# Kernel optimization log

Hardware: AMD Instinct MI355X
Metric: run time of the kernel (lower is better)

Reference implementation:

```python
import jax, jax.numpy as jnp
import numpy as np

INPUT_DIM = 512
LATENT_DIM = 64
H1, H2 = 128, 64  # hardcoded hidden widths in Encoder/Decoder
BATCH = 4096


def _xavier(key, shape):
    fan_out, fan_in = shape
    std = jnp.sqrt(2.0 / (fan_in + fan_out))
    return std * jax.random.normal(key, shape, dtype=jnp.float32)


def setup_inputs() -> dict:
    key = jax.random.key(0)
    ks = jax.random.split(key, 10)
    d = LATENT_DIM
    n_pairs = d * (d - 1) // 2
    n_funcs = 1 + d + n_pairs  # bias + states + pairwise products
    inp = {
        "x": jax.random.normal(ks[0], (BATCH, INPUT_DIM), dtype=jnp.float32),
        "xdot": jax.random.normal(ks[1], (BATCH, INPUT_DIM), dtype=jnp.float32),
        # encoder weights (torch Linear layout: [out, in])
        "We1": _xavier(ks[2], (H1, INPUT_DIM)), "be1": jnp.zeros((H1,), jnp.float32),
        "We2": _xavier(ks[3], (H2, H1)),        "be2": jnp.zeros((H2,), jnp.float32),
        "We3": _xavier(ks[4], (d, H2)),         "be3": jnp.zeros((d,), jnp.float32),
        # decoder weights
        "Wd1": _xavier(ks[5], (H2, d)),         "bd1": jnp.zeros((H2,), jnp.float32),
        "Wd2": _xavier(ks[6], (H1, H2)),        "bd2": jnp.zeros((H1,), jnp.float32),
        "Wd3": _xavier(ks[7], (INPUT_DIM, H1)), "bd3": jnp.zeros((INPUT_DIM,), jnp.float32),
        "XI": jnp.ones((n_funcs, d), jnp.float32),
        "XI_mask": jnp.ones((n_funcs, d), jnp.float32),
    }
    return inp


def _mlp_with_jacobian(x, Ws, bs):
    """3-layer relu MLP; returns output and per-sample analytic Jacobian [B,out,in].
    Jacobian = diag(m3) W3 diag(m2) W2 diag(m1) W1 with relu masks m_l."""
    h = x
    J = None
    for W, b in zip(Ws, bs):
        h = h @ W.T + b                      # [B, out_l]
        m = (h > 0).astype(h.dtype)          # relu mask (grad 0 at 0, matching torch)
        h = jnp.maximum(h, 0)
        Wm = m[:, :, None] * W[None]         # [B, out_l, in_l]
        J = Wm if J is None else jnp.einsum('boh,bhi->boi', Wm, J)
    return h, J


def _sindy_library(z):
    B, d = z.shape
    iu, ju = np.triu_indices(d, k=1)
    ones = jnp.ones((B, 1), z.dtype)
    pairs = z[:, iu] * z[:, ju]              # [B, d(d-1)/2]
    return jnp.concatenate([ones, z, pairs], axis=1)


def reference(x, xdot, We1, be1, We2, be2, We3, be3,
              Wd1, bd1, Wd2, bd2, Wd3, bd3, XI, XI_mask):
    z, Jenc = _mlp_with_jacobian(x, (We1, We2, We3), (be1, be2, be3))
    dz_dt = jnp.einsum('bli,bi->bl', Jenc, xdot)
    xh, Jdec = _mlp_with_jacobian(z, (Wd1, Wd2, Wd3), (bd1, bd2, bd3))
    theta = _sindy_library(z)
    dz_dt_sindy = theta @ (XI_mask * XI)
    dxh_dt = jnp.einsum('bol,bl->bo', Jdec, dz_dt_sindy)
    return (xh, dxh_dt, z, dz_dt, dz_dt_sindy)
```

## Files before the change

### kernel.cpp

```cpp
#include <hip/hip_runtime.h>

#define BATCH 4096
#define IN_DIM 512
#define H1DIM 128
#define H2DIM 64
#define DDIM 64
#define NFUNC 2081
#define NFPAD 2112
#define CHUNK 704
#define KS_PER_CHUNK 22

typedef short bf16x8 __attribute__((ext_vector_type(8)));
typedef float f32x4 __attribute__((ext_vector_type(4)));
#define MFMA(a,b,c) __builtin_amdgcn_mfma_f32_16x16x32_bf16(a,b,c,0,0,0)

#define WSZ1 (H1DIM*IN_DIM)
#define WSZ2 (H2DIM*H1DIM)
#define WSZ3 (DDIM*H2DIM)
#define WSZ4 (H2DIM*DDIM)
#define WSZ5 (H1DIM*H2DIM)
#define WSZ6 (IN_DIM*H1DIM)

__device__ __forceinline__ short f2b(float f) {
    union { float f; unsigned u; } x; x.f = f;
    unsigned r = x.u + 0x7fffu + ((x.u >> 16) & 1u);
    return (short)(r >> 16);
}
__device__ __forceinline__ float b2f(short s) {
    union { unsigned u; float f; } x; x.u = ((unsigned)(unsigned short)s) << 16;
    return x.f;
}
__device__ __forceinline__ void split3f(float v, short& s0, short& s1, short& s2) {
    s0 = f2b(v); float r = v - b2f(s0);
    s1 = f2b(r); float r2 = r - b2f(s1);
    s2 = f2b(r2);
}
__device__ __forceinline__ uint2 pk4(const short* s) {
    union { short s[4]; uint2 u; } z;
    z.s[0] = s[0]; z.s[1] = s[1]; z.s[2] = s[2]; z.s[3] = s[3];
    return z.u;
}

template<int N> __device__ __forceinline__ void waitv() {
    asm volatile("s_waitcnt vmcnt(%0)" :: "n"(N) : "memory");
    __builtin_amdgcn_sched_barrier(0);
}

__device__ __forceinline__ void st_b16(short* t, int RS, int r, int c, short v) {
    int b = (c * 2) ^ ((r & 7) << 4);
    *(short*)((char*)(t + r * RS) + b) = v;
}
__device__ __forceinline__ void st_b64(short* t, int RS, int r, int c0, uint2 v) {
    int b = (c0 * 2) ^ ((r & 7) << 4);
    *(uint2*)((char*)(t + r * RS) + b) = v;
}
__device__ __forceinline__ bf16x8 ld_af(const short* t, int RS, int lane, int kbase) {
    int r = lane & 15;
    int b = ((kbase + (lane >> 4) * 8) * 2) ^ ((r & 7) << 4);
    return *(const bf16x8*)((const char*)(t + r * RS) + b);
}
__device__ __forceinline__ bf16x8 ld_bp(const short* P, int blk, int lane) {
    return *(const bf16x8*)(P + ((size_t)blk * 64 + lane) * 8);
}

__device__ __forceinline__ void mf9(bf16x8 f0, bf16x8 f1, bf16x8 f2, bf16x8 fv,
                                    bf16x8 b0, bf16x8 b1, bf16x8 b2,
                                    f32x4& P, f32x4& Q, f32x4& V) {
    P = MFMA(f0, b0, P); Q = MFMA(f1, b1, Q);
    P = MFMA(f1, b0, P); Q = MFMA(f0, b1, Q);
    P = MFMA(f2, b0, P); Q = MFMA(f2, b1, Q);
    P = MFMA(f0, b2, P); Q = MFMA(f1, b2, Q);
    V = MFMA(fv, b0, V);
}

__device__ __forceinline__ void epi_store(short* t0, short* t1, short* t2, short* tv, int RS,
                                          int lane, int col, const f32x4& P, const f32x4& Q,
                                          const f32x4& V, float bb)
{
    #pragma unroll
    for (int q = 0; q < 4; ++q) {
        int row = (lane >> 4) * 4 + q;
        float pre = P[q] + Q[q] + bb;
        float h = fmaxf(pre, 0.f);
        short s0, s1, s2;
        split3f(h, s0, s1, s2);
        st_b16(t0, RS, row, col, s0);
        st_b16(t1, RS, row, col, s1);
        st_b16(t2, RS, row, col, s2);
        st_b16(tv, RS, row, col, pre > 0.f ? f2b(V[q]) : (short)0);
    }
}

template<int K>
__device__ void pack_w(const float* __restrict__ W, short* __restrict__ dst, int NK,
                       int gid, int nthr)
{
    for (int i = gid; i < NK; i += nthr) {
        int c = i / K, k = i % K;
        int cb = c >> 4, ks = k >> 5;
        int L = (((k >> 3) & 3) << 4) | (c & 15);
        int j = k & 7;
        int idx = ((cb * (K / 32) + ks) * 64 + L) * 8 + j;
        short s0, s1, s2; split3f(W[i], s0, s1, s2);
        dst[idx] = s0; dst[idx + NK] = s1; dst[idx + 2 * NK] = s2;
    }
}

__global__ void initk(const float* __restrict__ x, const float* __restrict__ xdot,
                      const float* __restrict__ We1, const float* __restrict__ We2,
                      const float* __restrict__ We3, const float* __restrict__ Wd1,
                      const float* __restrict__ Wd2, const float* __restrict__ Wd3,
                      const float* __restrict__ XI, const float* __restrict__ XIm,
                      float* __restrict__ xh, float* __restrict__ dxh,
                      short* Wp1, short* Wp2, short* Wp3, short* Wp4, short* Wp5, short* Wp6,
                      short* xiP, int2* pk)
{
    int gid = blockIdx.x * blockDim.x + threadIdx.x;
    int nthr = gridDim.x * blockDim.x;

    for (int i = gid; i < (BATCH / 16) * 16 * 64; i += nthr) {
        int L = i & 63, ks = (i >> 6) & 15, rb = i >> 10;
        int row = rb * 16 + (L & 15);
        int k0 = ks * 32 + ((L >> 4) << 3);
        const float* px = &x[(size_t)row * IN_DIM + k0];
        const float* pd = &xdot[(size_t)row * IN_DIM + k0];
        union { short s[8]; bf16x8 v; } a0, a1, a2, dv;
        #pragma unroll
        for (int j = 0; j < 8; ++j) {
            split3f(px[j], a0.s[j], a1.s[j], a2.s[j]);
            dv.s[j] = f2b(pd[j]);
        }
        short* bx = (short*)(xh + (size_t)rb * 8192);
        short* bd = (short*)(dxh + (size_t)rb * 8192);
        int off = (ks * 64 + L) * 8;
        *(bf16x8*)(bx + off) = a0.v;
        *(bf16x8*)(bx + 8192 + off) = a1.v;
        *(bf16x8*)(bd + off) = a2.v;
        *(bf16x8*)(bd + 8192 + off) = dv.v;
    }

    pack_w<512>(We1, Wp1, WSZ1, gid, nthr);
    pack_w<128>(We2, Wp2, WSZ2, gid, nthr);
    pack_w<64>(We3, Wp3, WSZ3, gid, nthr);
    pack_w<64>(Wd1, Wp4, WSZ4, gid, nthr);
    pack_w<64>(Wd2, Wp5, WSZ5, gid, nthr);
    pack_w<128>(Wd3, Wp6, WSZ6, gid, nthr);

    for (int i = gid; i < 4 * 66 * 64; i += nthr) {
        int cb = i / (66 * 64);
        int r = i - cb * (66 * 64);
        int ks = r >> 6, L = r & 63;
        int col = cb * 16 + (L & 15);
        union { short s[8]; bf16x8 v; } w;
        #pragma unroll
        for (int j = 0; j < 8; ++j) {
            int f = ks * 32 + ((L >> 4) << 3) + j;
            float v = (f < NFUNC) ? XI[(size_t)f * DDIM + col] * XIm[(size_t)f * DDIM + col] : 0.f;
            w.s[j] = f2b(v);
        }
        *(bf16x8*)(xiP + (size_t)i * 8) = w.v;
    }

    for (int f = gid; f < NFPAD; f += nthr) {
        int a, b;
        if (f == 0) { a = 64; b = 64; }
        else if (f <= DDIM) { a = f - 1; b = 64; }
        else if (f < NFUNC) {
            int p = f - 1 - DDIM; int i2 = 0, cum = 0;
            while (cum + (63 - i2) <= p) { cum += 63 - i2; ++i2; }
            a = i2; b = i2 + 1 + (p - cum);
        } else { a = 65; b = 65; }
        pk[f] = make_int2(a, b);
    }
}

__global__ __launch_bounds__(256, 1)
void fused(const float* __restrict__ be1, const float* __restrict__ be2,
           const float* __restrict__ be3, const float* __restrict__ bd1,
           const float* __restrict__ bd2, const float* __restrict__ bd3,
           const short* __restrict__ Wp1, const short* __restrict__ Wp2,
           const short* __restrict__ Wp3, const short* __restrict__ Wp4,
           const short* __restrict__ Wp5, const short* __restrict__ Wp6,
           const short* __restrict__ xiP, const int2* __restrict__ pk,
           float* __restrict__ xh, float* __restrict__ dxh, float* __restrict__ zo,
           float* __restrict__ dz, float* __restrict__ dzs)
{
    __shared__ __align__(1024) char lds[122880];
#define GLL(gp, lo) __builtin_amdgcn_global_load_lds( \
        (const __attribute__((address_space(1))) unsigned int*)(gp), \
        (__attribute__((address_space(3))) unsigned int*)&lds[lo], 16, 0, 0)

    short* h1s0 = (short*)(lds + 0);
    short* h1s1 = (short*)(lds + 4096);
    short* h1s2 = (short*)(lds + 8192);
    short* v1   = (short*)(lds + 12288);
    short* h2s0 = (short*)(lds + 16384);
    short* h2s1 = (short*)(lds + 18432);
    short* h2s2 = (short*)(lds + 20480);
    short* v2   = (short*)(lds + 22528);
    short* th   = (short*)(lds + 0);
    short* g1s0 = (short*)(lds + 0);
    short* g1s1 = (short*)(lds + 2048);
    short* g1s2 = (short*)(lds + 4096);
    short* u1   = (short*)(lds + 6144);
    short* g2s0 = (short*)(lds + 8192);
    short* g2s1 = (short*)(lds + 12288);
    short* g2s2 = (short*)(lds + 16384);
    short* u2   = (short*)(lds + 20480);
    short* zb0  = (short*)(lds + 24576);
    short* zb1  = (short*)(lds + 26624);
    short* zb2  = (short*)(lds + 28672);
    short* dzsb = (short*)(lds + 30720);
    float* zf   = (float*)(lds + 32768);

    const int tid = threadIdx.x, lane = tid & 63, wave = tid >> 6;
    const int row0 = blockIdx.x * 16;
    const int c16 = lane & 15;
    const int lane16 = lane * 16;
    const int tr = tid & 15, tf44 = (tid >> 4) * 44;

    float bb1[2] = { be1[wave * 32 + c16], be1[wave * 32 + 16 + c16] };
    float bb2 = be2[wave * 16 + c16];
    float bb3 = be3[wave * 16 + c16];
    float bD1 = bd1[wave * 16 + c16];
    float bD2[2] = { bd2[wave * 32 + c16], bd2[wave * 32 + 16 + c16] };
    float bD3[8];
    #pragma unroll
    for (int i = 0; i < 8; ++i) bD3[i] = bd3[wave * 128 + i * 16 + c16];

    f32x4 P1[2] = {}, Q1[2] = {}, V1[2] = {};
    {
        const char* bxc = (const char*)(xh + (size_t)blockIdx.x * 8192);
        const char* bdc = (const char*)(dxh + (size_t)blockIdx.x * 8192);
        const char* w1ac = (const char*)Wp1;
        const char* w1bc = (const char*)(Wp1 + WSZ1);
        const char* w1cc = (const char*)(Wp1 + 2 * WSZ1);
#define SLOT1(d) (unsigned)(wave * 30720 + (d) * 10240)
#define ISS1(ks, d) { unsigned sb = SLOT1(d); \
        const char* ga = bxc + (ks) * 1024 + lane16; \
        GLL(ga, sb);            GLL(ga + 16384, sb + 1024); \
        const char* gd = bdc + (ks) * 1024 + lane16; \
        GLL(gd, sb + 2048);     GLL(gd + 16384, sb + 3072); \
        int bA = ((wave * 2) * 16 + (ks)) * 1024 + lane16; \
        int bB = ((wave * 2 + 1) * 16 + (ks)) * 1024 + lane16; \
        GLL(w1ac + bA, sb + 4096); GLL(w1bc + bA, sb + 5120); GLL(w1cc + bA, sb + 6144); \
        GLL(w1ac + bB, sb + 7168); GLL(w1bc + bB, sb + 8192); GLL(w1cc + bB, sb + 9216); }
#define STEP1(ks, WN) { waitv<WN>(); unsigned sb = SLOT1((ks) % 3); \
        bf16x8 f0  = *(const bf16x8*)&lds[sb + lane16]; \
        bf16x8 f1  = *(const bf16x8*)&lds[sb + 1024 + lane16]; \
        bf16x8 f2  = *(const bf16x8*)&lds[sb + 2048 + lane16]; \
        bf16x8 fv  = *(const bf16x8*)&lds[sb + 3072 + lane16]; \
        bf16x8 b00 = *(const bf16x8*)&lds[sb + 4096 + lane16]; \
        bf16x8 b01 = *(const bf16x8*)&lds[sb + 5120 + lane16]; \
        bf16x8 b02 = *(const bf16x8*)&lds[sb + 6144 + lane16]; \
        bf16x8 b10 = *(const bf16x8*)&lds[sb + 7168 + lane16]; \
        bf16x8 b11 = *(const bf16x8*)&lds[sb + 8192 + lane16]; \
        bf16x8 b12 = *(const bf16x8*)&lds[sb + 9216 + lane16]; \
        mf9(f0, f1, f2, fv, b00, b01, b02, P1[0], Q1[0], V1[0]); \
        mf9(f0, f1, f2, fv, b10, b11, b12, P1[1], Q1[1], V1[1]); \
        __builtin_amdgcn_sched_barrier(0); \
        if ((ks) + 3 < 16) ISS1((ks) + 3, (ks) % 3) }

        ISS1(0, 0) ISS1(1, 1) ISS1(2, 2)
        STEP1(0, 20)  STEP1(1, 20)  STEP1(2, 20)  STEP1(3, 20)
        STEP1(4, 20)  STEP1(5, 20)  STEP1(6, 20)  STEP1(7, 20)
        STEP1(8, 20)  STEP1(9, 20)  STEP1(10, 20) STEP1(11, 20)
        STEP1(12, 20) STEP1(13, 20) STEP1(14, 10) STEP1(15, 0)
#undef ISS1
#undef STEP1
#undef SLOT1
    }
    __syncthreads();
    #pragma unroll
    for (int nf = 0; nf < 2; ++nf) {
        int col = wave * 32 + nf * 16 + c16;
        epi_store(h1s0, h1s1, h1s2, v1, 128, lane, col, P1[nf], Q1[nf], V1[nf], bb1[nf]);
    }
    bf16x8 L2B[4][3];
    #pragma unroll
    for (int ks = 0; ks < 4; ++ks) {
        int blk = wave * 4 + ks;
        L2B[ks][0] = ld_bp(Wp2, blk, lane);
        L2B[ks][1] = ld_bp(Wp2 + WSZ2, blk, lane);
        L2B[ks][2] = ld_bp(Wp2 + 2 * WSZ2, blk, lane);
    }
    __syncthreads();

    bf16x8 L3B[2][3];
    {
        bf16x8 Aa[4][4];
        #pragma unroll
        for (int ks = 0; ks < 4; ++ks) {
            Aa[ks][0] = ld_af(h1s0, 128, lane, ks * 32);
            Aa[ks][1] = ld_af(h1s1, 128, lane, ks * 32);
            Aa[ks][2] = ld_af(h1s2, 128, lane, ks * 32);
            Aa[ks][3] = ld_af(v1, 128, lane, ks * 32);
        }
        #pragma unroll
        for (int ks = 0; ks < 2; ++ks) {
            int blk = wave * 2 + ks;
            L3B[ks][0] = ld_bp(Wp3, blk, lane);
            L3B[ks][1] = ld_bp(Wp3 + WSZ3, blk, lane);
            L3B[ks][2] = ld_bp(Wp3 + 2 * WSZ3, blk, lane);
        }
        f32x4 P = {}, Q = {}, V = {};
        #pragma unroll
        for (int ks = 0; ks < 4; ++ks)
            mf9(Aa[ks][0], Aa[ks][1], Aa[ks][2], Aa[ks][3], L2B[ks][0], L2B[ks][1], L2B[ks][2], P, Q, V);
        epi_store(h2s0, h2s1, h2s2, v2, 64, lane, wave * 16 + c16, P, Q, V, bb2);
    }
    __syncthreads();

    bf16x8 X[KS_PER_CHUNK];
    {
        bf16x8 Aa[2][4];
        #pragma unroll
        for (int ks = 0; ks < 2; ++ks) {
            Aa[ks][0] = ld_af(h2s0, 64, lane, ks * 32);
            Aa[ks][1] = ld_af(h2s1, 64, lane, ks * 32);
            Aa[ks][2] = ld_af(h2s2, 64, lane, ks * 32);
            Aa[ks][3] = ld_af(v2, 64, lane, ks * 32);
        }
        f32x4 P = {}, Q = {}, V = {};
        #pragma unroll
        for (int ks = 0; ks < 2; ++ks)
            mf9(Aa[ks][0], Aa[ks][1], Aa[ks][2], Aa[ks][3], L3B[ks][0], L3B[ks][1], L3B[ks][2], P, Q, V);
        #pragma unroll
        for (int kk = 0; kk < KS_PER_CHUNK; ++kk)
            X[kk] = ld_bp(xiP, wave * 66 + kk, lane);
        int col = wave * 16 + c16;
        #pragma unroll
        for (int q = 0; q < 4; ++q) {
            int row = (lane >> 4) * 4 + q;
            float pre = P[q] + Q[q] + bb3;
            float hz = fmaxf(pre, 0.f);
            float vz = pre > 0.f ? V[q] : 0.f;
            zf[row * 68 + col] = hz;
            short s0, s1, s2;
            split3f(hz, s0, s1, s2);
            st_b16(zb0, 64, row, col, s0);
            st_b16(zb1, 64, row, col, s1);
            st_b16(zb2, 64, row, col, s2);
            zo[(size_t)(row0 + row) * DDIM + col] = hz;
            dz[(size_t)(row0 + row) * DDIM + col] = vz;
        }
        if (tid < 32) { int r = tid & 15; zf[r * 68 + 64 + (tid >> 4)] = (tid >> 4) ? 0.f : 1.f; }
    }
    __syncthreads();

    f32x4 sa0 = {}, sa1 = {};
#define BUILD(ch) { _Pragma("unroll") for (int g = 0; g < 11; ++g) { \
        int fl = tf44 + g * 4, fg = (ch) * CHUNK + fl; \
        int4 qa = *(const int4*)&pk[fg]; int4 qb = *(const int4*)&pk[fg + 2]; \
        float t0 = zf[tr * 68 + qa.x] * zf[tr * 68 + qa.y]; \
        float t1 = zf[tr * 68 + qa.z] * zf[tr * 68 + qa.w]; \
        float t2 = zf[tr * 68 + qb.x] * zf[tr * 68 + qb.y]; \
        float t3 = zf[tr * 68 + qb.z] * zf[tr * 68 + qb.w]; \
        short arr[4] = { f2b(t0), f2b(t1), f2b(t2), f2b(t3) }; \
        st_b64(th, 704, tr, fl, pk4(arr)); } }
#define SMF() { _Pragma("unroll") for (int kk = 0; kk < KS_PER_CHUNK; ++kk) { \
        bf16x8 a = ld_af(th, 704, lane, kk * 32); \
        if (kk & 1) sa1 = MFMA(a, X[kk], sa1); else sa0 = MFMA(a, X[kk], sa0); } }
#define ISX(ch) { _Pragma("unroll") for (int kk = 0; kk < KS_PER_CHUNK; ++kk) \
        X[kk] = ld_bp(xiP, wave * 66 + (ch) * KS_PER_CHUNK + kk, lane); }

    BUILD(0)
    __syncthreads();
    SMF() ISX(1)
    __syncthreads();
    BUILD(1)
    __syncthreads();
    SMF() ISX(2)
    __syncthreads();
    BUILD(2)
    __syncthreads();
    SMF()
#undef BUILD
#undef SMF
#undef ISX
    bf16x8 D1B[2][3];
    {
        f32x4 sacc = sa0 + sa1;
        #pragma unroll
        for (int ks = 0; ks < 2; ++ks) {
            int blk = wave * 2 + ks;
            D1B[ks][0] = ld_bp(Wp4, blk, lane);
            D1B[ks][1] = ld_bp(Wp4 + WSZ4, blk, lane);
            D1B[ks][2] = ld_bp(Wp4 + 2 * WSZ4, blk, lane);
        }
        int col = wave * 16 + c16;
        #pragma unroll
        for (int q = 0; q < 4; ++q) {
            int row = (lane >> 4) * 4 + q;
            float v = sacc[q];
            dzs[(size_t)(row0 + row) * DDIM + col] = v;
            st_b16(dzsb, 64, row, col, f2b(v));
        }
    }
    __syncthreads();

    bf16x8 D2B[4][3];
    {
        bf16x8 Aa[2][4];
        #pragma unroll
        for (int ks = 0; ks < 2; ++ks) {
            Aa[ks][0] = ld_af(zb0, 64, lane, ks * 32);
            Aa[ks][1] = ld_af(zb1, 64, lane, ks * 32);
            Aa[ks][2] = ld_af(zb2, 64, lane, ks * 32);
            Aa[ks][3] = ld_af(dzsb, 64, lane, ks * 32);
        }
        #pragma unroll
        for (int cf = 0; cf < 2; ++cf)
            #pragma unroll
            for (int ks = 0; ks < 2; ++ks) {
                int blk = (wave * 2 + cf) * 2 + ks;
                D2B[cf * 2 + ks][0] = ld_bp(Wp5, blk, lane);
                D2B[cf * 2 + ks][1] = ld_bp(Wp5 + WSZ5, blk, lane);
                D2B[cf * 2 + ks][2] = ld_bp(Wp5 + 2 * WSZ5, blk, lane);
            }
        f32x4 P = {}, Q = {}, V = {};
        #pragma unroll
        for (int ks = 0; ks < 2; ++ks)
            mf9(Aa[ks][0], Aa[ks][1], Aa[ks][2], Aa[ks][3], D1B[ks][0], D1B[ks][1], D1B[ks][2], P, Q, V);
        epi_store(g1s0, g1s1, g1s2, u1, 64, lane, wave * 16 + c16, P, Q, V, bD1);
    }
    __syncthreads();

    {
        bf16x8 Aa[2][4];
        #pragma unroll
        for (int ks = 0; ks < 2; ++ks) {
            Aa[ks][0] = ld_af(g1s0, 64, lane, ks * 32);
            Aa[ks][1] = ld_af(g1s1, 64, lane, ks * 32);
            Aa[ks][2] = ld_af(g1s2, 64, lane, ks * 32);
            Aa[ks][3] = ld_af(u1, 64, lane, ks * 32);
        }
        f32x4 P[2] = {}, Q[2] = {}, V[2] = {};
        #pragma unroll
        for (int cf = 0; cf < 2; ++cf)
            #pragma unroll
            for (int ks = 0; ks < 2; ++ks)
                mf9(Aa[ks][0], Aa[ks][1], Aa[ks][2], Aa[ks][3],
                    D2B[cf * 2 + ks][0], D2B[cf * 2 + ks][1], D2B[cf * 2 + ks][2],
                    P[cf], Q[cf], V[cf]);
        #pragma unroll
        for (int cf = 0; cf < 2; ++cf) {
            int col = wave * 32 + cf * 16 + c16;
            epi_store(g2s0, g2s1, g2s2, u2, 128, lane, col, P[cf], Q[cf], V[cf], bD2[cf]);
        }
    }
    __syncthreads();

    bf16x8 Ax0, Ax1, Ax2, Axv;
    const char* w6ac = (const char*)Wp6;
    const char* w6bc = (const char*)(Wp6 + WSZ6);
    const char* w6cc = (const char*)(Wp6 + 2 * WSZ6);
#define D3SLOT(d) (unsigned)(40960 + wave * 12288 + (d) * 3072)
#define D3ISS(h, s) { unsigned sb = D3SLOT((s) & 3); \
        int bo = ((wave * 8 + (h) * 4 + ((s) & 3)) * 4 + ((s) >> 2)) * 1024 + lane16; \
        GLL(w6ac + bo, sb); GLL(w6bc + bo, sb + 1024); GLL(w6cc + bo, sb + 2048); }
#define D3STEP(h, s, WN, Pa, Qa, Va) { waitv<WN>(); \
        if (((s) & 3) == 0) { int ks = (s) >> 2; \
            Ax0 = ld_af(g2s0, 128, lane, ks * 32); Ax1 = ld_af(g2s1, 128, lane, ks * 32); \
            Ax2 = ld_af(g2s2, 128, lane, ks * 32); Axv = ld_af(u2, 128, lane, ks * 32); } \
        { unsigned sb = D3SLOT((s) & 3); \
          bf16x8 c0 = *(const bf16x8*)&lds[sb + lane16]; \
          bf16x8 c1 = *(const bf16x8*)&lds[sb + 1024 + lane16]; \
          bf16x8 c2 = *(const bf16x8*)&lds[sb + 2048 + lane16]; \
          mf9(Ax0, Ax1, Ax2, Axv, c0, c1, c2, Pa[(s) & 3], Qa[(s) & 3], Va[(s) & 3]); } \
        __builtin_amdgcn_sched_barrier(0); \
        if ((s) + 4 < 16) D3ISS(h, (s) + 4) }
#define D3EPI(h, P_, Q_, V_) { _Pragma("unroll") for (int cf = 0; cf < 4; ++cf) { \
        int col = wave * 128 + (h) * 64 + cf * 16 + c16; \
        float bb = bD3[(h) * 4 + cf]; \
        _Pragma("unroll") for (int q = 0; q < 4; ++q) { \
            int row = (lane >> 4) * 4 + q; \
            float pre = P_[cf][q] + Q_[cf][q] + bb; \
            xh[(size_t)(row0 + row) * IN_DIM + col] = fmaxf(pre, 0.f); \
            dxh[(size_t)(row0 + row) * IN_DIM + col] = pre > 0.f ? V_[cf][q] : 0.f; } } }

    {
        f32x4 P[4] = {}, Q[4] = {}, V[4] = {};
        D3ISS(0, 0) D3ISS(0, 1) D3ISS(0, 2) D3ISS(0, 3)
        D3STEP(0, 0, 9, P, Q, V)  D3STEP(0, 1, 9, P, Q, V)  D3STEP(0, 2, 9, P, Q, V)  D3STEP(0, 3, 9, P, Q, V)
        D3STEP(0, 4, 9, P, Q, V)  D3STEP(0, 5, 9, P, Q, V)  D3STEP(0, 6, 9, P, Q, V)  D3STEP(0, 7, 9, P, Q, V)
        D3STEP(0, 8, 9, P, Q, V)  D3STEP(0, 9, 9, P, Q, V)  D3STEP(0, 10, 9, P, Q, V) D3STEP(0, 11, 9, P, Q, V)
        D3STEP(0, 12, 9, P, Q, V) D3STEP(0, 13, 6, P, Q, V) D3STEP(0, 14, 3, P, Q, V) D3STEP(0, 15, 0, P, Q, V)
        D3EPI(0, P, Q, V)
    }
    {
        f32x4 P[4] = {}, Q[4] = {}, V[4] = {};
        D3ISS(1, 0) D3ISS(1, 1) D3ISS(1, 2) D3ISS(1, 3)
        D3STEP(1, 0, 9, P, Q, V)  D3STEP(1, 1, 9, P, Q, V)  D3STEP(1, 2, 9, P, Q, V)  D3STEP(1, 3, 9, P, Q, V)
        D3STEP(1, 4, 9, P, Q, V)  D3STEP(1, 5, 9, P, Q, V)  D3STEP(1, 6, 9, P, Q, V)  D3STEP(1, 7, 9, P, Q, V)
        D3STEP(1, 8, 9, P, Q, V)  D3STEP(1, 9, 9, P, Q, V)  D3STEP(1, 10, 9, P, Q, V) D3STEP(1, 11, 9, P, Q, V)
        D3STEP(1, 12, 9, P, Q, V) D3STEP(1, 13, 6, P, Q, V) D3STEP(1, 14, 3, P, Q, V) D3STEP(1, 15, 0, P, Q, V)
        D3EPI(1, P, Q, V)
    }
#undef D3ISS
#undef D3STEP
#undef D3EPI
#undef D3SLOT
#undef GLL
}

extern "C" void kernel_launch(void* const* d_in, const int* in_sizes, int n_in,
                              void* d_out, int out_size, void* d_ws, size_t ws_size,
                              hipStream_t stream)
{
    const float* x    = (const float*)d_in[0];
    const float* xdot = (const float*)d_in[1];
    const float* We1  = (const float*)d_in[2];
    const float* be1  = (const float*)d_in[3];
    const float* We2  = (const float*)d_in[4];
    const float* be2  = (const float*)d_in[5];
    const float* We3  = (const float*)d_in[6];
    const float* be3  = (const float*)d_in[7];
    const float* Wd1  = (const float*)d_in[8];
    const float* bd1  = (const float*)d_in[9];
    const float* Wd2  = (const float*)d_in[10];
    const float* bd2  = (const float*)d_in[11];
    const float* Wd3  = (const float*)d_in[12];
    const float* bd3  = (const float*)d_in[13];
    const float* XI   = (const float*)d_in[14];
    const float* XIm  = (const float*)d_in[15];

    float* out = (float*)d_out;
    float* xh  = out;
    float* dxh = out + (size_t)BATCH * IN_DIM;
    float* zo  = dxh + (size_t)BATCH * IN_DIM;
    float* dz  = zo + (size_t)BATCH * DDIM;
    float* dzs = dz + (size_t)BATCH * DDIM;

    int2*  pk  = (int2*)d_ws;
    short* Wp1 = (short*)(pk + NFPAD);
    short* Wp2 = Wp1 + 3 * WSZ1;
    short* Wp3 = Wp2 + 3 * WSZ2;
    short* Wp4 = Wp3 + 3 * WSZ3;
    short* Wp5 = Wp4 + 3 * WSZ4;
    short* Wp6 = Wp5 + 3 * WSZ5;
    short* xiP = Wp6 + 3 * WSZ6;

    initk<<<1024, 256, 0, stream>>>(x, xdot, We1, We2, We3, Wd1, Wd2, Wd3, XI, XIm,
                                    xh, dxh, Wp1, Wp2, Wp3, Wp4, Wp5, Wp6, xiP, pk);
    fused<<<BATCH / 16, 256, 0, stream>>>(be1, be2, be3, bd1, bd2, bd3,
                                          Wp1, Wp2, Wp3, Wp4, Wp5, Wp6, xiP, pk,
                                          xh, dxh, zo, dz, dzs);
}
```

Before: 48.65 us.

## Shrink LDS and registers for two blocks per CU, vectorize init packing

The fused kernel's LDS footprint drops from 120KB to 80KB by moving the layer-1 pipeline from triple to double buffering and relocating the decoder-3 staging slots. Fully unrolled macro sequences become non-unrolled loops, and the bd3 bias is loaded late instead of held in registers. Launch bounds now request two blocks per CU, so more waves can hide memory latency. The init kernel's weight and input packing now uses vectorized loads and 16-byte stores. The trade-off is a shallower prefetch depth per block and loop overhead in place of straight-line code.

```diff
diff --git a/kernel.cpp b/kernel.cpp
--- a/kernel.cpp
+++ b/kernel.cpp
@@ -95,14 +95,18 @@
 __device__ void pack_w(const float* __restrict__ W, short* __restrict__ dst, int NK,
                        int gid, int nthr)
 {
-    for (int i = gid; i < NK; i += nthr) {
-        int c = i / K, k = i % K;
-        int cb = c >> 4, ks = k >> 5;
-        int L = (((k >> 3) & 3) << 4) | (c & 15);
-        int j = k & 7;
-        int idx = ((cb * (K / 32) + ks) * 64 + L) * 8 + j;
-        short s0, s1, s2; split3f(W[i], s0, s1, s2);
-        dst[idx] = s0; dst[idx + NK] = s1; dst[idx + 2 * NK] = s2;
+    for (int o = gid; o < NK / 8; o += nthr) {
+        int c = o / (K / 8), k0 = (o - c * (K / 8)) * 8;
+        int cb = c >> 4, ks = k0 >> 5;
+        int L = (((k0 >> 3) & 3) << 4) | (c & 15);
+        int idx = ((cb * (K / 32) + ks) * 64 + L) * 8;
+        union { short s[8]; bf16x8 v; } p0, p1, p2;
+        #pragma unroll
+        for (int j = 0; j < 8; ++j)
+            split3f(W[(size_t)c * K + k0 + j], p0.s[j], p1.s[j], p2.s[j]);
+        *(bf16x8*)(dst + idx) = p0.v;
+        *(bf16x8*)(dst + NK + idx) = p1.v;
+        *(bf16x8*)(dst + 2 * NK + idx) = p2.v;
     }
 }
 
@@ -124,11 +128,14 @@
         int k0 = ks * 32 + ((L >> 4) << 3);
         const float* px = &x[(size_t)row * IN_DIM + k0];
         const float* pd = &xdot[(size_t)row * IN_DIM + k0];
+        f32x4 xa = *(const f32x4*)px, xb = *(const f32x4*)(px + 4);
+        f32x4 da = *(const f32x4*)pd, db = *(const f32x4*)(pd + 4);
         union { short s[8]; bf16x8 v; } a0, a1, a2, dv;
         #pragma unroll
-        for (int j = 0; j < 8; ++j) {
-            split3f(px[j], a0.s[j], a1.s[j], a2.s[j]);
-            dv.s[j] = f2b(pd[j]);
+        for (int j = 0; j < 4; ++j) {
+            split3f(xa[j], a0.s[j], a1.s[j], a2.s[j]);
+            split3f(xb[j], a0.s[j + 4], a1.s[j + 4], a2.s[j + 4]);
+            dv.s[j] = f2b(da[j]); dv.s[j + 4] = f2b(db[j]);
         }
         short* bx = (short*)(xh + (size_t)rb * 8192);
         short* bd = (short*)(dxh + (size_t)rb * 8192);
@@ -174,7 +181,7 @@
     }
 }
 
-__global__ __launch_bounds__(256, 1)
+__global__ __launch_bounds__(256, 2)
 void fused(const float* __restrict__ be1, const float* __restrict__ be2,
            const float* __restrict__ be3, const float* __restrict__ bd1,
            const float* __restrict__ bd2, const float* __restrict__ bd3,
@@ -185,7 +192,7 @@
            float* __restrict__ xh, float* __restrict__ dxh, float* __restrict__ zo,
            float* __restrict__ dz, float* __restrict__ dzs)
 {
-    __shared__ __align__(1024) char lds[122880];
+    __shared__ __align__(1024) char lds[81920];
 #define GLL(gp, lo) __builtin_amdgcn_global_load_lds( \
         (const __attribute__((address_space(1))) unsigned int*)(gp), \
         (__attribute__((address_space(3))) unsigned int*)&lds[lo], 16, 0, 0)
@@ -219,56 +226,57 @@
     const int lane16 = lane * 16;
     const int tr = tid & 15, tf44 = (tid >> 4) * 44;
 
+    const char* bxc = (const char*)(xh + (size_t)blockIdx.x * 8192);
+    const char* bdc = (const char*)(dxh + (size_t)blockIdx.x * 8192);
+    const char* w1ac = (const char*)Wp1;
+    const char* w1bc = (const char*)(Wp1 + WSZ1);
+    const char* w1cc = (const char*)(Wp1 + 2 * WSZ1);
+
     float bb1[2] = { be1[wave * 32 + c16], be1[wave * 32 + 16 + c16] };
     float bb2 = be2[wave * 16 + c16];
     float bb3 = be3[wave * 16 + c16];
     float bD1 = bd1[wave * 16 + c16];
     float bD2[2] = { bd2[wave * 32 + c16], bd2[wave * 32 + 16 + c16] };
-    float bD3[8];
-    #pragma unroll
-    for (int i = 0; i < 8; ++i) bD3[i] = bd3[wave * 128 + i * 16 + c16];
 
     f32x4 P1[2] = {}, Q1[2] = {}, V1[2] = {};
     {
-        const char* bxc = (const char*)(xh + (size_t)blockIdx.x * 8192);
-        const char* bdc = (const char*)(dxh + (size_t)blockIdx.x * 8192);
-        const char* w1ac = (const char*)Wp1;
-        const char* w1bc = (const char*)(Wp1 + WSZ1);
-        const char* w1cc = (const char*)(Wp1 + 2 * WSZ1);
-#define SLOT1(d) (unsigned)(wave * 30720 + (d) * 10240)
-#define ISS1(ks, d) { unsigned sb = SLOT1(d); \
-        const char* ga = bxc + (ks) * 1024 + lane16; \
-        GLL(ga, sb);            GLL(ga + 16384, sb + 1024); \
-        const char* gd = bdc + (ks) * 1024 + lane16; \
-        GLL(gd, sb + 2048);     GLL(gd + 16384, sb + 3072); \
-        int bA = ((wave * 2) * 16 + (ks)) * 1024 + lane16; \
-        int bB = ((wave * 2 + 1) * 16 + (ks)) * 1024 + lane16; \
-        GLL(w1ac + bA, sb + 4096); GLL(w1bc + bA, sb + 5120); GLL(w1cc + bA, sb + 6144); \
-        GLL(w1ac + bB, sb + 7168); GLL(w1bc + bB, sb + 8192); GLL(w1cc + bB, sb + 9216); }
-#define STEP1(ks, WN) { waitv<WN>(); unsigned sb = SLOT1((ks) % 3); \
-        bf16x8 f0  = *(const bf16x8*)&lds[sb + lane16]; \
-        bf16x8 f1  = *(const bf16x8*)&lds[sb + 1024 + lane16]; \
-        bf16x8 f2  = *(const bf16x8*)&lds[sb + 2048 + lane16]; \
-        bf16x8 fv  = *(const bf16x8*)&lds[sb + 3072 + lane16]; \
-        bf16x8 b00 = *(const bf16x8*)&lds[sb + 4096 + lane16]; \
-        bf16x8 b01 = *(const bf16x8*)&lds[sb + 5120 + lane16]; \
-        bf16x8 b02 = *(const bf16x8*)&lds[sb + 6144 + lane16]; \
-        bf16x8 b10 = *(const bf16x8*)&lds[sb + 7168 + lane16]; \
-        bf16x8 b11 = *(const bf16x8*)&lds[sb + 8192 + lane16]; \
-        bf16x8 b12 = *(const bf16x8*)&lds[sb + 9216 + lane16]; \
-        mf9(f0, f1, f2, fv, b00, b01, b02, P1[0], Q1[0], V1[0]); \
-        mf9(f0, f1, f2, fv, b10, b11, b12, P1[1], Q1[1], V1[1]); \
-        __builtin_amdgcn_sched_barrier(0); \
-        if ((ks) + 3 < 16) ISS1((ks) + 3, (ks) % 3) }
-
-        ISS1(0, 0) ISS1(1, 1) ISS1(2, 2)
-        STEP1(0, 20)  STEP1(1, 20)  STEP1(2, 20)  STEP1(3, 20)
-        STEP1(4, 20)  STEP1(5, 20)  STEP1(6, 20)  STEP1(7, 20)
-        STEP1(8, 20)  STEP1(9, 20)  STEP1(10, 20) STEP1(11, 20)
-        STEP1(12, 20) STEP1(13, 20) STEP1(14, 10) STEP1(15, 0)
-#undef ISS1
-#undef STEP1
-#undef SLOT1
+        const unsigned slotb = wave * 20480;
+        auto iss1 = [&](int ks, int d) {
+            unsigned sb = slotb + d * 10240;
+            const char* ga = bxc + ks * 1024 + lane16;
+            GLL(ga, sb);            GLL(ga + 16384, sb + 1024);
+            const char* gd = bdc + ks * 1024 + lane16;
+            GLL(gd, sb + 2048);     GLL(gd + 16384, sb + 3072);
+            int bA = ((wave * 2) * 16 + ks) * 1024 + lane16;
+            int bB = ((wave * 2 + 1) * 16 + ks) * 1024 + lane16;
+            GLL(w1ac + bA, sb + 4096); GLL(w1bc + bA, sb + 5120); GLL(w1cc + bA, sb + 6144);
+            GLL(w1ac + bB, sb + 7168); GLL(w1bc + bB, sb + 8192); GLL(w1cc + bB, sb + 9216);
+        };
+        auto step1 = [&](int ks) {
+            unsigned sb = slotb + (ks & 1) * 10240;
+            bf16x8 f0  = *(const bf16x8*)&lds[sb + lane16];
+            bf16x8 f1  = *(const bf16x8*)&lds[sb + 1024 + lane16];
+            bf16x8 f2  = *(const bf16x8*)&lds[sb + 2048 + lane16];
+            bf16x8 fv  = *(const bf16x8*)&lds[sb + 3072 + lane16];
+            bf16x8 b00 = *(const bf16x8*)&lds[sb + 4096 + lane16];
+            bf16x8 b01 = *(const bf16x8*)&lds[sb + 5120 + lane16];
+            bf16x8 b02 = *(const bf16x8*)&lds[sb + 6144 + lane16];
+            bf16x8 b10 = *(const bf16x8*)&lds[sb + 7168 + lane16];
+            bf16x8 b11 = *(const bf16x8*)&lds[sb + 8192 + lane16];
+            bf16x8 b12 = *(const bf16x8*)&lds[sb + 9216 + lane16];
+            mf9(f0, f1, f2, fv, b00, b01, b02, P1[0], Q1[0], V1[0]);
+            mf9(f0, f1, f2, fv, b10, b11, b12, P1[1], Q1[1], V1[1]);
+            __builtin_amdgcn_sched_barrier(0);
+        };
+        iss1(0, 0); iss1(1, 1);
+        #pragma clang loop unroll(disable)
+        for (int ks = 0; ks < 14; ++ks) {
+            waitv<10>();
+            step1(ks);
+            iss1(ks + 2, ks & 1);
+        }
+        waitv<10>(); step1(14);
+        waitv<0>();  step1(15);
     }
     __syncthreads();
     #pragma unroll
@@ -349,33 +357,37 @@
     __syncthreads();
 
     f32x4 sa0 = {}, sa1 = {};
-#define BUILD(ch) { _Pragma("unroll") for (int g = 0; g < 11; ++g) { \
-        int fl = tf44 + g * 4, fg = (ch) * CHUNK + fl; \
-        int4 qa = *(const int4*)&pk[fg]; int4 qb = *(const int4*)&pk[fg + 2]; \
-        float t0 = zf[tr * 68 + qa.x] * zf[tr * 68 + qa.y]; \
-        float t1 = zf[tr * 68 + qa.z] * zf[tr * 68 + qa.w]; \
-        float t2 = zf[tr * 68 + qb.x] * zf[tr * 68 + qb.y]; \
-        float t3 = zf[tr * 68 + qb.z] * zf[tr * 68 + qb.w]; \
-        short arr[4] = { f2b(t0), f2b(t1), f2b(t2), f2b(t3) }; \
-        st_b64(th, 704, tr, fl, pk4(arr)); } }
+    auto build = [&](int ch) {
+        #pragma clang loop unroll(disable)
+        for (int g = 0; g < 11; ++g) {
+            int fl = tf44 + g * 4, fg = ch * CHUNK + fl;
+            int4 qa = *(const int4*)&pk[fg];
+            int4 qb = *(const int4*)&pk[fg + 2];
+            float t0 = zf[tr * 68 + qa.x] * zf[tr * 68 + qa.y];
+            float t1 = zf[tr * 68 + qa.z] * zf[tr * 68 + qa.w];
+            float t2 = zf[tr * 68 + qb.x] * zf[tr * 68 + qb.y];
+            float t3 = zf[tr * 68 + qb.z] * zf[tr * 68 + qb.w];
+            short arr[4] = { f2b(t0), f2b(t1), f2b(t2), f2b(t3) };
+            st_b64(th, 704, tr, fl, pk4(arr));
+        }
+    };
 #define SMF() { _Pragma("unroll") for (int kk = 0; kk < KS_PER_CHUNK; ++kk) { \
         bf16x8 a = ld_af(th, 704, lane, kk * 32); \
         if (kk & 1) sa1 = MFMA(a, X[kk], sa1); else sa0 = MFMA(a, X[kk], sa0); } }
 #define ISX(ch) { _Pragma("unroll") for (int kk = 0; kk < KS_PER_CHUNK; ++kk) \
         X[kk] = ld_bp(xiP, wave * 66 + (ch) * KS_PER_CHUNK + kk, lane); }
 
-    BUILD(0)
+    build(0);
     __syncthreads();
     SMF() ISX(1)
     __syncthreads();
-    BUILD(1)
+    build(1);
     __syncthreads();
     SMF() ISX(2)
     __syncthreads();
-    BUILD(2)
+    build(2);
     __syncthreads();
     SMF()
-#undef BUILD
 #undef SMF
 #undef ISX
     bf16x8 D1B[2][3];
@@ -451,56 +463,57 @@
     }
     __syncthreads();
 
-    bf16x8 Ax0, Ax1, Ax2, Axv;
-    const char* w6ac = (const char*)Wp6;
-    const char* w6bc = (const char*)(Wp6 + WSZ6);
-    const char* w6cc = (const char*)(Wp6 + 2 * WSZ6);
-#define D3SLOT(d) (unsigned)(40960 + wave * 12288 + (d) * 3072)
-#define D3ISS(h, s) { unsigned sb = D3SLOT((s) & 3); \
-        int bo = ((wave * 8 + (h) * 4 + ((s) & 3)) * 4 + ((s) >> 2)) * 1024 + lane16; \
-        GLL(w6ac + bo, sb); GLL(w6bc + bo, sb + 1024); GLL(w6cc + bo, sb + 2048); }
-#define D3STEP(h, s, WN, Pa, Qa, Va) { waitv<WN>(); \
-        if (((s) & 3) == 0) { int ks = (s) >> 2; \
-            Ax0 = ld_af(g2s0, 128, lane, ks * 32); Ax1 = ld_af(g2s1, 128, lane, ks * 32); \
-            Ax2 = ld_af(g2s2, 128, lane, ks * 32); Axv = ld_af(u2, 128, lane, ks * 32); } \
-        { unsigned sb = D3SLOT((s) & 3); \
-          bf16x8 c0 = *(const bf16x8*)&lds[sb + lane16]; \
-          bf16x8 c1 = *(const bf16x8*)&lds[sb + 1024 + lane16]; \
-          bf16x8 c2 = *(const bf16x8*)&lds[sb + 2048 + lane16]; \
-          mf9(Ax0, Ax1, Ax2, Axv, c0, c1, c2, Pa[(s) & 3], Qa[(s) & 3], Va[(s) & 3]); } \
-        __builtin_amdgcn_sched_barrier(0); \
-        if ((s) + 4 < 16) D3ISS(h, (s) + 4) }
-#define D3EPI(h, P_, Q_, V_) { _Pragma("unroll") for (int cf = 0; cf < 4; ++cf) { \
-        int col = wave * 128 + (h) * 64 + cf * 16 + c16; \
-        float bb = bD3[(h) * 4 + cf]; \
-        _Pragma("unroll") for (int q = 0; q < 4; ++q) { \
-            int row = (lane >> 4) * 4 + q; \
-            float pre = P_[cf][q] + Q_[cf][q] + bb; \
-            xh[(size_t)(row0 + row) * IN_DIM + col] = fmaxf(pre, 0.f); \
-            dxh[(size_t)(row0 + row) * IN_DIM + col] = pre > 0.f ? V_[cf][q] : 0.f; } } }
-
-    {
-        f32x4 P[4] = {}, Q[4] = {}, V[4] = {};
-        D3ISS(0, 0) D3ISS(0, 1) D3ISS(0, 2) D3ISS(0, 3)
-        D3STEP(0, 0, 9, P, Q, V)  D3STEP(0, 1, 9, P, Q, V)  D3STEP(0, 2, 9, P, Q, V)  D3STEP(0, 3, 9, P, Q, V)
-        D3STEP(0, 4, 9, P, Q, V)  D3STEP(0, 5, 9, P, Q, V)  D3STEP(0, 6, 9, P, Q, V)  D3STEP(0, 7, 9, P, Q, V)
-        D3STEP(0, 8, 9, P, Q, V)  D3STEP(0, 9, 9, P, Q, V)  D3STEP(0, 10, 9, P, Q, V) D3STEP(0, 11, 9, P, Q, V)
-        D3STEP(0, 12, 9, P, Q, V) D3STEP(0, 13, 6, P, Q, V) D3STEP(0, 14, 3, P, Q, V) D3STEP(0, 15, 0, P, Q, V)
-        D3EPI(0, P, Q, V)
-    }
-    {
-        f32x4 P[4] = {}, Q[4] = {}, V[4] = {};
-        D3ISS(1, 0) D3ISS(1, 1) D3ISS(1, 2) D3ISS(1, 3)
-        D3STEP(1, 0, 9, P, Q, V)  D3STEP(1, 1, 9, P, Q, V)  D3STEP(1, 2, 9, P, Q, V)  D3STEP(1, 3, 9, P, Q, V)
-        D3STEP(1, 4, 9, P, Q, V)  D3STEP(1, 5, 9, P, Q, V)  D3STEP(1, 6, 9, P, Q, V)  D3STEP(1, 7, 9, P, Q, V)
-        D3STEP(1, 8, 9, P, Q, V)  D3STEP(1, 9, 9, P, Q, V)  D3STEP(1, 10, 9, P, Q, V) D3STEP(1, 11, 9, P, Q, V)
-        D3STEP(1, 12, 9, P, Q, V) D3STEP(1, 13, 6, P, Q, V) D3STEP(1, 14, 3, P, Q, V) D3STEP(1, 15, 0, P, Q, V)
-        D3EPI(1, P, Q, V)
-    }
-#undef D3ISS
-#undef D3STEP
-#undef D3EPI
-#undef D3SLOT
+    {
+        const char* w6ac = (const char*)Wp6;
+        const char* w6bc = (const char*)(Wp6 + WSZ6);
+        const char* w6cc = (const char*)(Wp6 + 2 * WSZ6);
+        const unsigned d3b = 24576 + wave * 12288;
+        #pragma clang loop unroll(disable)
+        for (int h = 0; h < 2; ++h) {
+            auto d3iss = [&](int s) {
+                unsigned sb = d3b + (s & 3) * 3072;
+                int bo = ((wave * 8 + h * 4 + (s & 3)) * 4 + (s >> 2)) * 1024 + lane16;
+                GLL(w6ac + bo, sb); GLL(w6bc + bo, sb + 1024); GLL(w6cc + bo, sb + 2048);
+            };
+            f32x4 P[4] = {}, Q[4] = {}, V[4] = {};
+            d3iss(0); d3iss(1); d3iss(2); d3iss(3);
+            bf16x8 Ax0, Ax1, Ax2, Axv;
+#define D3C(cf) { unsigned sb = d3b + (cf) * 3072; \
+            bf16x8 c0 = *(const bf16x8*)&lds[sb + lane16]; \
+            bf16x8 c1 = *(const bf16x8*)&lds[sb + 1024 + lane16]; \
+            bf16x8 c2 = *(const bf16x8*)&lds[sb + 2048 + lane16]; \
+            mf9(Ax0, Ax1, Ax2, Axv, c0, c1, c2, P[cf], Q[cf], V[cf]); \
+            __builtin_amdgcn_sched_barrier(0); }
+            #pragma clang loop unroll(disable)
+            for (int ks = 0; ks < 3; ++ks) {
+                Ax0 = ld_af(g2s0, 128, lane, ks * 32); Ax1 = ld_af(g2s1, 128, lane, ks * 32);
+                Ax2 = ld_af(g2s2, 128, lane, ks * 32); Axv = ld_af(u2, 128, lane, ks * 32);
+                waitv<9>(); D3C(0) d3iss(ks * 4 + 4);
+                waitv<9>(); D3C(1) d3iss(ks * 4 + 5);
+                waitv<9>(); D3C(2) d3iss(ks * 4 + 6);
+                waitv<9>(); D3C(3) d3iss(ks * 4 + 7);
+            }
+            Ax0 = ld_af(g2s0, 128, lane, 96); Ax1 = ld_af(g2s1, 128, lane, 96);
+            Ax2 = ld_af(g2s2, 128, lane, 96); Axv = ld_af(u2, 128, lane, 96);
+            waitv<9>(); D3C(0)
+            waitv<6>(); D3C(1)
+            waitv<3>(); D3C(2)
+            waitv<0>(); D3C(3)
+#undef D3C
+            #pragma unroll
+            for (int cf = 0; cf < 4; ++cf) {
+                int col = wave * 128 + h * 64 + cf * 16 + c16;
+                float bb = bd3[col];
+                #pragma unroll
+                for (int q = 0; q < 4; ++q) {
+                    int row = (lane >> 4) * 4 + q;
+                    float pre = P[cf][q] + Q[cf][q] + bb;
+                    xh[(size_t)(row0 + row) * IN_DIM + col] = fmaxf(pre, 0.f);
+                    dxh[(size_t)(row0 + row) * IN_DIM + col] = pre > 0.f ? V[cf][q] : 0.f;
+                }
+            }
+        }
+    }
 #undef GLL
 }
 
```

Result: slower. 52.39 us (+7.7%).
